# Performance work log

Hardware: AMD Instinct MI355X
Metric: run time of the kernel (lower is better)

Reference implementation:

```python
import jax, jax.numpy as jnp
import numpy as np

N_GENES = 2048   # col_dim: nodes of the PPI graph, feature dim of cols-SAGE
N_CELLS = 4096   # row_dim: nodes of the KNN graph, feature dim of rows-SAGE
E_KNN = 61440
E_PPI = 65536
INTER = 512
EMBD = 128
SLOPE = 0.01       # LeakyReLU default negative_slope
SCALE_PARAM = 3.0  # cols_encoder custom attention scale

_PARAM_SHAPES = [
    ("c0_wl", (N_GENES, N_GENES)), ("c0_wr", (N_GENES, N_GENES)), ("c0_b", (N_GENES,)),
    ("r0_wl", (N_CELLS, N_CELLS)), ("r0_wr", (N_CELLS, N_CELLS)), ("r0_b", (N_CELLS,)),
    ("c1_wl", (N_GENES, N_GENES)), ("c1_wr", (N_GENES, N_GENES)), ("c1_b", (N_GENES,)),
    ("r1_wl", (N_CELLS, N_CELLS)), ("r1_wr", (N_CELLS, N_CELLS)), ("r1_b", (N_CELLS,)),
    ("gr_w", (N_CELLS, INTER)), ("gr_b", (INTER,)),
    ("tr_wq", (INTER, EMBD)), ("tr_bq", (EMBD,)), ("tr_wk", (INTER, EMBD)), ("tr_bk", (EMBD,)),
    ("tr_wv", (INTER, EMBD)), ("tr_bv", (EMBD,)), ("tr_ws", (INTER, EMBD)), ("tr_bs", (EMBD,)),
    ("gc_w", (N_GENES, INTER)), ("gc_b", (INTER,)),
    ("tc_wq", (INTER, EMBD)), ("tc_bq", (EMBD,)), ("tc_wk", (INTER, EMBD)), ("tc_bk", (EMBD,)),
    ("tc_wv", (INTER, EMBD)), ("tc_bv", (EMBD,)), ("tc_ws", (INTER, EMBD)), ("tc_bs", (EMBD,)),
    ("d1_w", (EMBD, INTER)), ("d1_b", (INTER,)),
    ("d2_w", (INTER, INTER)), ("d2_b", (INTER,)),
    ("d3_w", (INTER, N_GENES)), ("d3_b", (N_GENES,)),
]


def setup_inputs() -> dict:
    key = jax.random.key(0)
    ki = iter(jax.random.split(key, 64))
    inp = {
        "x": jax.random.normal(next(ki), (N_GENES, N_CELLS), jnp.float32),
        "knn_edge_index": jax.random.randint(next(ki), (2, E_KNN), 0, N_CELLS, dtype=jnp.int32),
        "ppi_edge_index": jax.random.randint(next(ki), (2, E_PPI), 0, N_GENES, dtype=jnp.int32),
    }
    for name, shape in _PARAM_SHAPES:
        scale = 1.0 / float(np.sqrt(shape[0])) if len(shape) == 2 else 0.01
        inp[name] = jax.random.normal(next(ki), shape, jnp.float32) * scale
    return inp


def _leaky(x):
    return jax.nn.leaky_relu(x, SLOPE)


def _gcn(x, ei, w, b):
    # GCNConv: add self loops, symmetric D^-1/2 (A+I) D^-1/2 normalization
    n = x.shape[0]
    loop = jnp.arange(n, dtype=ei.dtype)
    src = jnp.concatenate([ei[0], loop])
    dst = jnp.concatenate([ei[1], loop])
    deg = jax.ops.segment_sum(jnp.ones(src.shape, x.dtype), dst, n)
    dinv = jnp.where(deg > 0, jax.lax.rsqrt(jnp.maximum(deg, 1.0)), 0.0)
    h = x @ w
    msg = h[src] * (dinv[src] * dinv[dst])[:, None]
    return jax.ops.segment_sum(msg, dst, n) + b


def _sage(x, ei, wl, wr, b):
    # SAGEConv: mean neighbor aggregation -> lin_l, plus root lin_r
    n = x.shape[0]
    src, dst = ei[0], ei[1]
    s = jax.ops.segment_sum(x[src], dst, n)
    cnt = jax.ops.segment_sum(jnp.ones(src.shape, x.dtype), dst, n)
    agg = s / jnp.maximum(cnt, 1.0)[:, None]
    return agg @ wl + x @ wr + b


def _tconv(x, ei, wq, bq, wk, bk, wv, bv, ws, bs, scale_param):
    # TransformerConv (heads=1). scale_param=None -> per-target softmax;
    # otherwise the custom mean/std standardization + sigmoid (TransformerConvReducrLayer).
    n, d = x.shape[0], wq.shape[1]
    q = x @ wq + bq
    k = x @ wk + bk
    v = x @ wv + bv
    src, dst = ei[0], ei[1]
    alpha = jnp.sum(q[dst] * k[src], axis=-1) / jnp.sqrt(jnp.asarray(d, x.dtype))
    if scale_param is None:
        m = jax.ops.segment_max(alpha, dst, n)
        e = jnp.exp(alpha - m[dst])
        z = jax.ops.segment_sum(e, dst, n)
        a = e / jnp.where(z > 0, z, 1.0)[dst]
    else:
        mu = jnp.mean(alpha)
        sd = jnp.std(alpha, ddof=1)  # torch.std is unbiased
        a = jax.nn.sigmoid((alpha - mu) / ((1.0 / scale_param) * sd))
    out = jax.ops.segment_sum(a[:, None] * v[src], dst, n)
    return out + x @ ws + bs  # root skip (lin_skip)


def reference(x, knn_edge_index, ppi_edge_index,
              c0_wl, c0_wr, c0_b, r0_wl, r0_wr, r0_b,
              c1_wl, c1_wr, c1_b, r1_wl, r1_wr, r1_b,
              gr_w, gr_b, tr_wq, tr_bq, tr_wk, tr_bk, tr_wv, tr_bv, tr_ws, tr_bs,
              gc_w, gc_b, tc_wq, tc_bq, tc_wk, tc_bk, tc_wv, tc_bv, tc_ws, tc_bs,
              d1_w, d1_b, d2_w, d2_b, d3_w, d3_b):
    # dropout layers are identity at inference
    emb = x  # [genes, cells]
    for (cwl, cwr, cb, rwl, rwr, rb) in [
        (c0_wl, c0_wr, c0_b, r0_wl, r0_wr, r0_b),
        (c1_wl, c1_wr, c1_b, r1_wl, r1_wr, r1_b),
    ]:
        emb = _leaky(_sage(emb.T, knn_edge_index, cwl, cwr, cb)).T  # cells graph
        emb = _leaky(_sage(emb, ppi_edge_index, rwl, rwr, rb))      # genes graph
    # rows encoder: GCN + TransformerConv (softmax attention) over PPI graph
    hr = _leaky(_gcn(emb, ppi_edge_index, gr_w, gr_b))
    emb_rows = _tconv(hr, ppi_edge_index, tr_wq, tr_bq, tr_wk, tr_bk,
                      tr_wv, tr_bv, tr_ws, tr_bs, None)
    # cols encoder: GCN + reducer TransformerConv (sigmoid-standardized attention) over KNN graph
    hc = _leaky(_gcn(emb.T, knn_edge_index, gc_w, gc_b))
    emb_cols = _tconv(hc, knn_edge_index, tc_wq, tc_bq, tc_wk, tc_bk,
                      tc_wv, tc_bv, tc_ws, tc_bs, SCALE_PARAM)
    # feature decoder MLP
    h = jax.nn.relu(emb_cols @ d1_w + d1_b)
    h = jax.nn.relu(h @ d2_w + d2_b)
    out_features = h @ d3_w + d3_b
    return (emb_rows, emb_cols, out_features)
```

## Files before the change

### kernel.cpp

```cpp
#include <hip/hip_runtime.h>
#include <math.h>

#define NG 2048
#define NC 4096
#define EKNN 61440
#define EPPI 65536

typedef __attribute__((ext_vector_type(8))) short short8v;
typedef __attribute__((ext_vector_type(4))) float f32x4;
typedef unsigned short ushort_t;

static inline int cdiv(int a, int b) { return (a + b - 1) / b; }

__device__ __forceinline__ unsigned short f2b(float f) {
    union { float f; unsigned int i; } v; v.f = f;
    unsigned int r = v.i + 0x7FFFu + ((v.i >> 16) & 1u);
    return (unsigned short)(r >> 16);
}
__device__ __forceinline__ float bl(unsigned int u) { union { unsigned int i; float f; } v; v.i = u << 16; return v.f; }
__device__ __forceinline__ float bh(unsigned int u) { union { unsigned int i; float f; } v; v.i = u & 0xFFFF0000u; return v.f; }
__device__ __forceinline__ unsigned int pk2(float a, float b) { return (unsigned int)f2b(a) | ((unsigned int)f2b(b) << 16); }

__device__ __forceinline__ int xcd_swz_id() {
    const int nwg = gridDim.x * gridDim.y;
    const int orig = blockIdx.y * gridDim.x + blockIdx.x;
    const int q = nwg >> 3, r = nwg & 7;
    const int xcd = orig & 7, off = orig >> 3;
    return (xcd < r ? xcd * (q + 1) : r * (q + 1) + (xcd - r) * q) + off;
}

#define GLOAD_LDS16(gp, lp) __builtin_amdgcn_global_load_lds( \
    (const __attribute__((address_space(1))) void*)(gp),      \
    (__attribute__((address_space(3))) void*)(lp), 16, 0, 0)

template<int ACT, bool BIAS, bool OBF>
__global__ __launch_bounds__(256)
void gemm_bf16(const ushort_t* __restrict__ A,
               const ushort_t* __restrict__ Bt,
               const float* __restrict__ bias,
               float* __restrict__ Cf, ushort_t* __restrict__ Cb,
               int M, int N, int K) {
    __shared__ ushort_t lds[2][2][128 * 32];
    const int tid = threadIdx.x;
    const int lane = tid & 63, wv = tid >> 6;
    const int wm = wv >> 1, wn = wv & 1;
    const int swzid = xcd_swz_id();
    const int bm = (swzid / gridDim.x) << 7, bn = (swzid % gridDim.x) << 7;

    const ushort_t* gA = A + (size_t)bm * K;
    const ushort_t* gB = Bt + (size_t)bn * K;

    const int rsub = lane >> 2;
    const int qsw  = (lane & 3) ^ ((lane >> 3) & 3);
    const int KT = K >> 5;

    f32x4 acc[4][4];
    #pragma unroll
    for (int i = 0; i < 4; ++i)
        #pragma unroll
        for (int j = 0; j < 4; ++j) acc[i][j] = (f32x4){0.f, 0.f, 0.f, 0.f};

    auto stage = [&](int buf, int k0) {
        #pragma unroll
        for (int t = 0; t < 2; ++t) {
            const int br = (wv * 2 + t) * 16;
            GLOAD_LDS16(gA + (size_t)(br + rsub) * K + k0 + qsw * 8, &lds[buf][0][br * 32]);
            GLOAD_LDS16(gB + (size_t)(br + rsub) * K + k0 + qsw * 8, &lds[buf][1][br * 32]);
        }
    };

    const int rl = lane & 15, kg = lane >> 4;
    const int swr = (kg ^ ((rl >> 1) & 3)) * 8;

    stage(0, 0);
    int buf = 0;
    for (int kt = 0; kt < KT; ++kt) {
        __syncthreads();
        if (kt + 1 < KT) stage(buf ^ 1, (kt + 1) << 5);
        short8v a[4], b[4];
        #pragma unroll
        for (int mi = 0; mi < 4; ++mi)
            a[mi] = *(const short8v*)&lds[buf][0][(wm * 64 + mi * 16 + rl) * 32 + swr];
        #pragma unroll
        for (int ni = 0; ni < 4; ++ni)
            b[ni] = *(const short8v*)&lds[buf][1][(wn * 64 + ni * 16 + rl) * 32 + swr];
        #pragma unroll
        for (int mi = 0; mi < 4; ++mi)
            #pragma unroll
            for (int ni = 0; ni < 4; ++ni)
                acc[mi][ni] = __builtin_amdgcn_mfma_f32_16x16x32_bf16(a[mi], b[ni], acc[mi][ni], 0, 0, 0);
        buf ^= 1;
    }

    const int colL = lane & 15, rq = lane >> 4;
    #pragma unroll
    for (int mi = 0; mi < 4; ++mi) {
        const int row0 = bm + wm * 64 + mi * 16 + rq * 4;
        #pragma unroll
        for (int ni = 0; ni < 4; ++ni) {
            const int col = bn + wn * 64 + ni * 16 + colL;
            float bv = 0.f;
            if (BIAS) bv = bias[col];
            #pragma unroll
            for (int r = 0; r < 4; ++r) {
                const size_t off = (size_t)(row0 + r) * N + col;
                float v = acc[mi][ni][r];
                if (BIAS) v += bv;
                if (ACT == 2) v = fmaxf(v, 0.f);
                if (OBF) Cb[off] = f2b(v); else Cf[off] = v;
            }
        }
    }
}

__global__ __launch_bounds__(256)
void gemm_sage(const ushort_t* __restrict__ A0, const ushort_t* __restrict__ B0t,
               const ushort_t* __restrict__ A1, const ushort_t* __restrict__ B1t,
               const float* __restrict__ bias, ushort_t* __restrict__ Cb,
               int M, int N, int K) {
    __shared__ ushort_t lds[2][2][128 * 32];
    const int tid = threadIdx.x;
    const int lane = tid & 63, wv = tid >> 6;
    const int wm = wv >> 1, wn = wv & 1;
    const int swzid = xcd_swz_id();
    const int bm = (swzid / gridDim.x) << 7, bn = (swzid % gridDim.x) << 7;

    const ushort_t* gA0 = A0 + (size_t)bm * K;
    const ushort_t* gB0 = B0t + (size_t)bn * K;
    const ushort_t* gA1 = A1 + (size_t)bm * K;
    const ushort_t* gB1 = B1t + (size_t)bn * K;

    const int rsub = lane >> 2;
    const int qsw  = (lane & 3) ^ ((lane >> 3) & 3);
    const int KT = K >> 5;

    f32x4 acc[4][4];
    #pragma unroll
    for (int i = 0; i < 4; ++i)
        #pragma unroll
        for (int j = 0; j < 4; ++j) acc[i][j] = (f32x4){0.f, 0.f, 0.f, 0.f};

    auto stage = [&](int buf, int kt) {
        const int half = kt >= KT;
        const int k0 = (half ? (kt - KT) : kt) << 5;
        const ushort_t* sA = half ? gA1 : gA0;
        const ushort_t* sB = half ? gB1 : gB0;
        #pragma unroll
        for (int t = 0; t < 2; ++t) {
            const int br = (wv * 2 + t) * 16;
            GLOAD_LDS16(sA + (size_t)(br + rsub) * K + k0 + qsw * 8, &lds[buf][0][br * 32]);
            GLOAD_LDS16(sB + (size_t)(br + rsub) * K + k0 + qsw * 8, &lds[buf][1][br * 32]);
        }
    };

    const int rl = lane & 15, kg = lane >> 4;
    const int swr = (kg ^ ((rl >> 1) & 3)) * 8;

    stage(0, 0);
    int buf = 0;
    const int KT2 = KT * 2;
    for (int kt = 0; kt < KT2; ++kt) {
        __syncthreads();
        if (kt + 1 < KT2) stage(buf ^ 1, kt + 1);
        short8v a[4], b[4];
        #pragma unroll
        for (int mi = 0; mi < 4; ++mi)
            a[mi] = *(const short8v*)&lds[buf][0][(wm * 64 + mi * 16 + rl) * 32 + swr];
        #pragma unroll
        for (int ni = 0; ni < 4; ++ni)
            b[ni] = *(const short8v*)&lds[buf][1][(wn * 64 + ni * 16 + rl) * 32 + swr];
        #pragma unroll
        for (int mi = 0; mi < 4; ++mi)
            #pragma unroll
            for (int ni = 0; ni < 4; ++ni)
                acc[mi][ni] = __builtin_amdgcn_mfma_f32_16x16x32_bf16(a[mi], b[ni], acc[mi][ni], 0, 0, 0);
        buf ^= 1;
    }

    const int colL = lane & 15, rq = lane >> 4;
    #pragma unroll
    for (int mi = 0; mi < 4; ++mi) {
        const int row0 = bm + wm * 64 + mi * 16 + rq * 4;
        float bz[4];
        #pragma unroll
        for (int r = 0; r < 4; ++r) bz[r] = bias[row0 + r];
        #pragma unroll
        for (int ni = 0; ni < 4; ++ni) {
            const int col = bn + wn * 64 + ni * 16 + colL;
            #pragma unroll
            for (int r = 0; r < 4; ++r) {
                float v = acc[mi][ni][r] + bz[r];
                v = v > 0.f ? v : 0.01f * v;
                Cb[(size_t)(row0 + r) * N + col] = f2b(v);
            }
        }
    }
}

__global__ __launch_bounds__(256)
void transpose_f2b(const float* __restrict__ in, ushort_t* __restrict__ out, int R, int C) {
    __shared__ ushort_t t[64][65];
    const int bx = blockIdx.x << 6, by = blockIdx.y << 6;
    const int tr = threadIdx.x >> 4;
    const int tc = (threadIdx.x & 15) << 2;
    #pragma unroll
    for (int i = 0; i < 4; ++i) {
        const int rr = tr + i * 16;
        const float4 v = *(const float4*)(in + (size_t)(by + rr) * C + bx + tc);
        t[rr][tc + 0] = f2b(v.x); t[rr][tc + 1] = f2b(v.y);
        t[rr][tc + 2] = f2b(v.z); t[rr][tc + 3] = f2b(v.w);
    }
    __syncthreads();
    #pragma unroll
    for (int i = 0; i < 4; ++i) {
        const int cc = tr + i * 16;
        ushort4 o;
        o.x = t[tc + 0][cc]; o.y = t[tc + 1][cc];
        o.z = t[tc + 2][cc]; o.w = t[tc + 3][cc];
        *(ushort4*)(out + (size_t)(bx + cc) * R + by + tc) = o;
    }
}

__global__ __launch_bounds__(256)
void transpose_b2b(const ushort_t* __restrict__ in, ushort_t* __restrict__ out, int R, int C) {
    __shared__ ushort_t t[64][65];
    const int bx = blockIdx.x << 6, by = blockIdx.y << 6;
    const int tr = threadIdx.x >> 4;
    const int tc = (threadIdx.x & 15) << 2;
    #pragma unroll
    for (int i = 0; i < 4; ++i) {
        const int rr = tr + i * 16;
        const ushort4 v = *(const ushort4*)(in + (size_t)(by + rr) * C + bx + tc);
        t[rr][tc + 0] = v.x; t[rr][tc + 1] = v.y;
        t[rr][tc + 2] = v.z; t[rr][tc + 3] = v.w;
    }
    __syncthreads();
    #pragma unroll
    for (int i = 0; i < 4; ++i) {
        const int cc = tr + i * 16;
        ushort4 o;
        o.x = t[tc + 0][cc]; o.y = t[tc + 1][cc];
        o.z = t[tc + 2][cc]; o.w = t[tc + 3][cc];
        *(ushort4*)(out + (size_t)(bx + cc) * R + by + tc) = o;
    }
}

__global__ __launch_bounds__(256)
void transpose_qkvs(const float* __restrict__ wq, const float* __restrict__ wk,
                    const float* __restrict__ wv, const float* __restrict__ wsk,
                    ushort_t* __restrict__ out) {
    const float* in = blockIdx.z == 0 ? wq : blockIdx.z == 1 ? wk : blockIdx.z == 2 ? wv : wsk;
    ushort_t* o = out + (size_t)blockIdx.z * 128 * 512;
    __shared__ ushort_t t[64][65];
    const int bx = blockIdx.x << 6, by = blockIdx.y << 6;
    const int tr = threadIdx.x >> 4;
    const int tc = (threadIdx.x & 15) << 2;
    #pragma unroll
    for (int i = 0; i < 4; ++i) {
        const int rr = tr + i * 16;
        const float4 v = *(const float4*)(in + (size_t)(by + rr) * 128 + bx + tc);
        t[rr][tc + 0] = f2b(v.x); t[rr][tc + 1] = f2b(v.y);
        t[rr][tc + 2] = f2b(v.z); t[rr][tc + 3] = f2b(v.w);
    }
    __syncthreads();
    #pragma unroll
    for (int i = 0; i < 4; ++i) {
        const int cc = tr + i * 16;
        ushort4 ov;
        ov.x = t[tc + 0][cc]; ov.y = t[tc + 1][cc];
        ov.z = t[tc + 2][cc]; ov.w = t[tc + 3][cc];
        *(ushort4*)(o + (size_t)(bx + cc) * 512 + by + tc) = ov;
    }
}

__global__ void count_dst(const int* __restrict__ dst, float* __restrict__ cnt, int E) {
    int e = blockIdx.x * blockDim.x + threadIdx.x;
    if (e < E) atomicAdd(&cnt[dst[e]], 1.0f);
}

__global__ void make_dinv(const float* __restrict__ cnt, float* __restrict__ dinv, int n) {
    int i = blockIdx.x * blockDim.x + threadIdx.x;
    if (i < n) dinv[i] = rsqrtf(cnt[i] + 1.0f);
}

__global__ __launch_bounds__(256)
void scan_rowptr(const float* __restrict__ cnt, int* __restrict__ rowptr, int n) {
    __shared__ int part[257];
    const int tid = threadIdx.x;
    const int per = n >> 8;
    const int base = tid * per;
    int s = 0;
    for (int i = 0; i < per; ++i) s += (int)cnt[base + i];
    part[tid + 1] = s;
    if (tid == 0) part[0] = 0;
    __syncthreads();
    if (tid == 0)
        for (int i = 1; i <= 256; ++i) part[i] += part[i - 1];
    __syncthreads();
    int run = part[tid];
    for (int i = 0; i < per; ++i) {
        rowptr[base + i] = run;
        run += (int)cnt[base + i];
    }
    if (tid == 255) rowptr[n] = run;
}

__global__ void fill_csr(const int* __restrict__ src, const int* __restrict__ dst,
                         const int* __restrict__ rowptr, int* __restrict__ cursor,
                         int* __restrict__ srcs, int* __restrict__ eids, int E) {
    int e = blockIdx.x * blockDim.x + threadIdx.x;
    if (e >= E) return;
    int d = dst[e];
    int p = atomicAdd(&cursor[d], 1);
    int idx = rowptr[d] + p;
    srcs[idx] = src[e];
    eids[idx] = e;
}

__global__ void concat4(const float* __restrict__ a, const float* __restrict__ b,
                        const float* __restrict__ c, const float* __restrict__ d,
                        float* __restrict__ o) {
    int i = threadIdx.x + blockIdx.x * blockDim.x;
    if (i >= 512) return;
    float v;
    if (i < 128) v = a[i];
    else if (i < 256) v = b[i - 128];
    else if (i < 384) v = c[i - 256];
    else v = d[i - 384];
    o[i] = v;
}

template<int NS>
__global__ __launch_bounds__(256)
void sage_gather_b(const int* __restrict__ rowptr, const int* __restrict__ srcs,
                   const ushort_t* __restrict__ x, ushort_t* __restrict__ out) {
    const int F = NS * 2048;
    const int node = blockIdx.x, tid = threadIdx.x;
    const int beg = rowptr[node], end = rowptr[node + 1];
    __shared__ int snb[256];
    float acc[NS][8];
    #pragma unroll
    for (int s = 0; s < NS; ++s)
        #pragma unroll
        for (int j = 0; j < 8; ++j) acc[s][j] = 0.f;
    for (int c = beg; c < end; c += 256) {
        const int m = min(256, end - c);
        __syncthreads();
        if (tid < m) snb[tid] = srcs[c + tid];
        __syncthreads();
        #pragma unroll 2
        for (int i = 0; i < m; ++i) {
            const uint4* row = (const uint4*)(x + (size_t)snb[i] * F);
            #pragma unroll
            for (int s = 0; s < NS; ++s) {
                const uint4 v = row[tid + s * 256];
                acc[s][0] += bl(v.x); acc[s][1] += bh(v.x);
                acc[s][2] += bl(v.y); acc[s][3] += bh(v.y);
                acc[s][4] += bl(v.z); acc[s][5] += bh(v.z);
                acc[s][6] += bl(v.w); acc[s][7] += bh(v.w);
            }
        }
    }
    const float inv = 1.f / fmaxf((float)(end - beg), 1.f);
    uint4* orow = (uint4*)(out + (size_t)node * F);
    #pragma unroll
    for (int s = 0; s < NS; ++s) {
        uint4 o;
        o.x = pk2(acc[s][0] * inv, acc[s][1] * inv);
        o.y = pk2(acc[s][2] * inv, acc[s][3] * inv);
        o.z = pk2(acc[s][4] * inv, acc[s][5] * inv);
        o.w = pk2(acc[s][6] * inv, acc[s][7] * inv);
        orow[tid + s * 256] = o;
    }
}

__global__ __launch_bounds__(128)
void gcn_gather_b(const int* __restrict__ rowptr, const int* __restrict__ srcs,
                  const float* __restrict__ h, const float* __restrict__ dinv,
                  const float* __restrict__ b, ushort_t* __restrict__ out) {
    const int node = blockIdx.x, tid = threadIdx.x;
    const int beg = rowptr[node], end = rowptr[node + 1];
    __shared__ int snb[128];
    __shared__ float sdi[128];
    float ax = 0.f, ay = 0.f, az = 0.f, aw = 0.f;
    for (int c = beg; c < end; c += 128) {
        const int m = min(128, end - c);
        __syncthreads();
        if (tid < m) { int s = srcs[c + tid]; snb[tid] = s; sdi[tid] = dinv[s]; }
        __syncthreads();
        for (int i = 0; i < m; ++i) {
            const float4 v = ((const float4*)(h + (size_t)snb[i] * 512))[tid];
            const float w = sdi[i];
            ax += v.x * w; ay += v.y * w; az += v.z * w; aw += v.w * w;
        }
    }
    const float dd = dinv[node];
    const float4 hv = ((const float4*)(h + (size_t)node * 512))[tid];
    const float4 bv = ((const float4*)b)[tid];
    float4 o;
    o.x = ax * dd + hv.x * dd * dd + bv.x;
    o.y = ay * dd + hv.y * dd * dd + bv.y;
    o.z = az * dd + hv.z * dd * dd + bv.z;
    o.w = aw * dd + hv.w * dd * dd + bv.w;
    o.x = o.x > 0.f ? o.x : 0.01f * o.x;
    o.y = o.y > 0.f ? o.y : 0.01f * o.y;
    o.z = o.z > 0.f ? o.z : 0.01f * o.z;
    o.w = o.w > 0.f ? o.w : 0.01f * o.w;
    ((uint2*)(out + (size_t)node * 512))[tid] = make_uint2(pk2(o.x, o.y), pk2(o.z, o.w));
}

__global__ __launch_bounds__(128)
void tconv_softmax_gather(const int* __restrict__ rowptr, const int* __restrict__ srcs,
                          const int* __restrict__ eids, const float* __restrict__ alpha,
                          const float* __restrict__ qkvs, float* __restrict__ out) {
    const int node = blockIdx.x, tid = threadIdx.x;
    const int beg = rowptr[node], end = rowptr[node + 1];
    __shared__ int snb[128];
    __shared__ float sa[128];
    float mx = -INFINITY;
    for (int c = beg; c < end; c += 128) {
        const int m = min(128, end - c);
        __syncthreads();
        if (tid < m) sa[tid] = alpha[eids[c + tid]];
        __syncthreads();
        for (int i = 0; i < m; ++i) mx = fmaxf(mx, sa[i]);
    }
    float acc = 0.f, z = 0.f;
    for (int c = beg; c < end; c += 128) {
        const int m = min(128, end - c);
        __syncthreads();
        if (tid < m) { snb[tid] = srcs[c + tid]; sa[tid] = __expf(alpha[eids[c + tid]] - mx); }
        __syncthreads();
        for (int i = 0; i < m; ++i) {
            z += sa[i];
            acc += sa[i] * qkvs[(size_t)snb[i] * 512 + 256 + tid];
        }
    }
    const float r = acc * (z > 0.f ? 1.f / z : 0.f) + qkvs[(size_t)node * 512 + 384 + tid];
    out[(size_t)node * 128 + tid] = r;
}

template<bool WB16>
__global__ __launch_bounds__(128)
void tconv_sigmoid_gather(const int* __restrict__ rowptr, const int* __restrict__ srcs,
                          const int* __restrict__ eids, const float* __restrict__ alpha,
                          const float* __restrict__ qkvs, const double* __restrict__ stats,
                          float scale_param, int E, float* __restrict__ out,
                          ushort_t* __restrict__ ob) {
    const int node = blockIdx.x, tid = threadIdx.x;
    const int beg = rowptr[node], end = rowptr[node + 1];
    const double sum = stats[0], sumsq = stats[1];
    const double mu = sum / (double)E;
    const double var = (sumsq - sum * sum / (double)E) / (double)(E - 1);
    const float sd = (float)sqrt(fmax(var, 0.0));
    const float kk = scale_param / sd;
    const float fmu = (float)mu;
    __shared__ int snb[128];
    __shared__ float sa[128];
    float acc = 0.f;
    for (int c = beg; c < end; c += 128) {
        const int m = min(128, end - c);
        __syncthreads();
        if (tid < m) {
            snb[tid] = srcs[c + tid];
            const float t = (alpha[eids[c + tid]] - fmu) * kk;
            sa[tid] = 1.f / (1.f + __expf(-t));
        }
        __syncthreads();
        for (int i = 0; i < m; ++i)
            acc += sa[i] * qkvs[(size_t)snb[i] * 512 + 256 + tid];
    }
    const float r = acc + qkvs[(size_t)node * 512 + 384 + tid];
    out[(size_t)node * 128 + tid] = r;
    if (WB16) ob[(size_t)node * 128 + tid] = f2b(r);
}

__global__ __launch_bounds__(256)
void edge_dot_s(const int* __restrict__ src, const int* __restrict__ dst,
                const float* __restrict__ qkvs, float* __restrict__ alpha, int E) {
    int wid = (blockIdx.x * blockDim.x + threadIdx.x) >> 6;
    int lane = threadIdx.x & 63;
    if (wid >= E) return;
    const size_t qb = (size_t)dst[wid] * 512;
    const size_t kb = (size_t)src[wid] * 512 + 128;
    float v = qkvs[qb + lane] * qkvs[kb + lane]
            + qkvs[qb + 64 + lane] * qkvs[kb + 64 + lane];
    #pragma unroll
    for (int off = 32; off; off >>= 1) v += __shfl_down(v, off);
    if (lane == 0) alpha[wid] = v * 0.08838834764831845f;
}

__global__ __launch_bounds__(256)
void reduce_stats(const float* __restrict__ a, int E, double* __restrict__ stats) {
    double s = 0.0, s2 = 0.0;
    for (int i = blockIdx.x * blockDim.x + threadIdx.x; i < E; i += gridDim.x * blockDim.x) {
        double x = a[i];
        s += x; s2 += x * x;
    }
    #pragma unroll
    for (int off = 32; off; off >>= 1) {
        s += __shfl_down(s, off);
        s2 += __shfl_down(s2, off);
    }
    __shared__ double sh[4][2];
    int w = threadIdx.x >> 6;
    if ((threadIdx.x & 63) == 0) { sh[w][0] = s; sh[w][1] = s2; }
    __syncthreads();
    if (threadIdx.x == 0) {
        double t = sh[0][0] + sh[1][0] + sh[2][0] + sh[3][0];
        double t2 = sh[0][1] + sh[1][1] + sh[2][1] + sh[3][1];
        atomicAdd(&stats[0], t);
        atomicAdd(&stats[1], t2);
    }
}

static constexpr size_t NBIG = (size_t)NG * NC;
static constexpr size_t NBH = NBIG / 2;
static constexpr size_t OFF_B1 = 0;
static constexpr size_t OFF_B2 = NBH;
static constexpr size_t OFF_B3 = 2 * NBH;
static constexpr size_t OFF_WBF = 3 * NBH;
static constexpr size_t OFF_H1   = OFF_WBF + 2097152;
static constexpr size_t OFF_H2B  = OFF_H1 + (size_t)4096 * 512;
static constexpr size_t OFF_H3B  = OFF_H2B + (size_t)4096 * 512 / 2;
static constexpr size_t OFF_QKVS = OFF_H3B + (size_t)4096 * 512 / 2;
static constexpr size_t OFF_CBF  = OFF_QKVS + (size_t)4096 * 512;
static constexpr size_t OFF_B4 = OFF_WBF + 2 * NBIG;
static constexpr size_t OFF_ALPHA = OFF_B4 + 512;
static constexpr size_t OFF_CNTK = OFF_ALPHA + 65536;
static constexpr size_t OFF_CNTP = OFF_CNTK + 4096;
static constexpr size_t OFF_DINVK = OFF_CNTP + 4096;
static constexpr size_t OFF_DINVP = OFF_DINVK + 4096;
static constexpr size_t OFF_STATS = OFF_DINVP + 4096;
static constexpr size_t OFF_RPK = OFF_STATS + 16;
static constexpr size_t OFF_RPP = OFF_RPK + 4112;
static constexpr size_t OFF_SRCK = OFF_RPP + 2064;
static constexpr size_t OFF_EIDK = OFF_SRCK + EKNN;
static constexpr size_t OFF_SRCP = OFF_EIDK + EKNN;
static constexpr size_t OFF_EIDP = OFF_SRCP + EPPI;
static constexpr size_t OFF_CUR = OFF_EIDP + EPPI;

extern "C" void kernel_launch(void* const* d_in, const int* in_sizes, int n_in,
                              void* d_out, int out_size, void* d_ws, size_t ws_size,
                              hipStream_t stream) {
    const float* x      = (const float*)d_in[0];
    const int*   knn    = (const int*)d_in[1];
    const int*   ppi    = (const int*)d_in[2];
    const float* c0_wl = (const float*)d_in[3],  *c0_wr = (const float*)d_in[4],  *c0_b = (const float*)d_in[5];
    const float* r0_wl = (const float*)d_in[6],  *r0_wr = (const float*)d_in[7],  *r0_b = (const float*)d_in[8];
    const float* c1_wl = (const float*)d_in[9],  *c1_wr = (const float*)d_in[10], *c1_b = (const float*)d_in[11];
    const float* r1_wl = (const float*)d_in[12], *r1_wr = (const float*)d_in[13], *r1_b = (const float*)d_in[14];
    const float* gr_w  = (const float*)d_in[15], *gr_b  = (const float*)d_in[16];
    const float* tr_wq = (const float*)d_in[17], *tr_bq = (const float*)d_in[18];
    const float* tr_wk = (const float*)d_in[19], *tr_bk = (const float*)d_in[20];
    const float* tr_wv = (const float*)d_in[21], *tr_bv = (const float*)d_in[22];
    const float* tr_ws = (const float*)d_in[23], *tr_bs = (const float*)d_in[24];
    const float* gc_w  = (const float*)d_in[25], *gc_b  = (const float*)d_in[26];
    const float* tc_wq = (const float*)d_in[27], *tc_bq = (const float*)d_in[28];
    const float* tc_wk = (const float*)d_in[29], *tc_bk = (const float*)d_in[30];
    const float* tc_wv = (const float*)d_in[31], *tc_bv = (const float*)d_in[32];
    const float* tc_ws = (const float*)d_in[33], *tc_bs = (const float*)d_in[34];
    const float* d1_w  = (const float*)d_in[35], *d1_b  = (const float*)d_in[36];
    const float* d2_w  = (const float*)d_in[37], *d2_b  = (const float*)d_in[38];
    const float* d3_w  = (const float*)d_in[39], *d3_b  = (const float*)d_in[40];

    const int* knn_src = knn, *knn_dst = knn + EKNN;
    const int* ppi_src = ppi, *ppi_dst = ppi + EPPI;

    float* ws = (float*)d_ws;
    ushort_t* B1 = (ushort_t*)(ws + OFF_B1);
    ushort_t* B2 = (ushort_t*)(ws + OFF_B2);
    ushort_t* B3 = (ushort_t*)(ws + OFF_B3);
    ushort_t* WBF0 = (ushort_t*)(ws + OFF_WBF);
    ushort_t* WBF1 = WBF0 + 2 * NBIG;
    float* H1 = ws + OFF_H1;
    ushort_t* H2b = (ushort_t*)(ws + OFF_H2B);
    ushort_t* H3b = (ushort_t*)(ws + OFF_H3B);
    float* QKVS = ws + OFF_QKVS;
    ushort_t* CBF = (ushort_t*)(ws + OFF_CBF);
    float* B4 = ws + OFF_B4;
    float* ALPHA = ws + OFF_ALPHA;
    float* CNTK = ws + OFF_CNTK;
    float* CNTP = ws + OFF_CNTP;
    float* DINVK = ws + OFF_DINVK;
    float* DINVP = ws + OFF_DINVP;
    double* STATS = (double*)(ws + OFF_STATS);
    int* RPK  = (int*)(ws + OFF_RPK);
    int* RPP  = (int*)(ws + OFF_RPP);
    int* SRCK = (int*)(ws + OFF_SRCK);
    int* EIDK = (int*)(ws + OFF_EIDK);
    int* SRCP = (int*)(ws + OFF_SRCP);
    int* EIDP = (int*)(ws + OFF_EIDP);
    int* CUR  = (int*)(ws + OFF_CUR);

    float* out_rows = (float*)d_out;
    float* out_cols = out_rows + (size_t)NG * 128;
    float* out_feat = out_cols + (size_t)NC * 128;

    auto tW = [&](const float* Wsrc, int K, int N, ushort_t* dst) {
        transpose_f2b<<<dim3(N >> 6, K >> 6), 256, 0, stream>>>(Wsrc, dst, K, N);
    };
    auto gemm = [&](const ushort_t* Abf, const ushort_t* Wt, const float* bias,
                    float* Cf, ushort_t* Cb, int M, int N, int K, int mode) {
        dim3 g(N >> 7, M >> 7), blk(256);
        switch (mode) {
            case 0: gemm_bf16<0, false, false><<<g, blk, 0, stream>>>(Abf, Wt, nullptr, Cf, nullptr, M, N, K); break;
            case 2: gemm_bf16<0, true,  false><<<g, blk, 0, stream>>>(Abf, Wt, bias, Cf, nullptr, M, N, K); break;
            case 3: gemm_bf16<2, true,  true ><<<g, blk, 0, stream>>>(Abf, Wt, bias, nullptr, Cb, M, N, K); break;
        }
    };

    hipMemsetAsync(CNTK, 0, NC * 4, stream);
    hipMemsetAsync(CNTP, 0, NG * 4, stream);
    count_dst<<<cdiv(EKNN, 256), 256, 0, stream>>>(knn_dst, CNTK, EKNN);
    count_dst<<<cdiv(EPPI, 256), 256, 0, stream>>>(ppi_dst, CNTP, EPPI);
    make_dinv<<<cdiv(NC, 256), 256, 0, stream>>>(CNTK, DINVK, NC);
    make_dinv<<<cdiv(NG, 256), 256, 0, stream>>>(CNTP, DINVP, NG);
    scan_rowptr<<<1, 256, 0, stream>>>(CNTK, RPK, NC);
    scan_rowptr<<<1, 256, 0, stream>>>(CNTP, RPP, NG);
    hipMemsetAsync(CUR, 0, NC * 4, stream);
    fill_csr<<<cdiv(EKNN, 256), 256, 0, stream>>>(knn_src, knn_dst, RPK, CUR, SRCK, EIDK, EKNN);
    hipMemsetAsync(CUR, 0, NG * 4, stream);
    fill_csr<<<cdiv(EPPI, 256), 256, 0, stream>>>(ppi_src, ppi_dst, RPP, CUR, SRCP, EIDP, EPPI);

    transpose_f2b<<<dim3(NC >> 6, NG >> 6), 256, 0, stream>>>(x, B1, NG, NC);
    const float* cwl[2] = {c0_wl, c1_wl}; const float* cwr[2] = {c0_wr, c1_wr}; const float* cbb[2] = {c0_b, c1_b};
    const float* rwl[2] = {r0_wl, r1_wl}; const float* rwr[2] = {r0_wr, r1_wr}; const float* rbb[2] = {r0_b, r1_b};
    for (int l = 0; l < 2; ++l) {
        sage_gather_b<1><<<NC, 256, 0, stream>>>(RPK, SRCK, B1, B2);
        tW(cwl[l], NG, NG, WBF0);
        tW(cwr[l], NG, NG, WBF1);
        gemm_sage<<<dim3(NC >> 7, NG >> 7), 256, 0, stream>>>(WBF0, B2, WBF1, B1, cbb[l], B3, NG, NC, NG);
        sage_gather_b<2><<<NG, 256, 0, stream>>>(RPP, SRCP, B3, B2);
        tW(rwl[l], NC, NC, WBF0);
        tW(rwr[l], NC, NC, WBF1);
        gemm_sage<<<dim3(NG >> 7, NC >> 7), 256, 0, stream>>>(WBF0, B2, WBF1, B3, rbb[l], B1, NC, NG, NC);
    }
    transpose_b2b<<<dim3(NG >> 6, NC >> 6), 256, 0, stream>>>(B1, B3, NC, NG);

    tW(gr_w, NC, 512, WBF0);
    gemm(B3, WBF0, nullptr, H1, nullptr, NG, 512, NC, 0);
    gcn_gather_b<<<NG, 128, 0, stream>>>(RPP, SRCP, H1, DINVP, gr_b, H2b);
    transpose_qkvs<<<dim3(2, 8, 4), 256, 0, stream>>>(tr_wq, tr_wk, tr_wv, tr_ws, WBF0);
    concat4<<<2, 256, 0, stream>>>(tr_bq, tr_bk, tr_bv, tr_bs, B4);
    gemm(H2b, WBF0, B4, QKVS, nullptr, NG, 512, 512, 2);
    edge_dot_s<<<cdiv(EPPI * 64, 256), 256, 0, stream>>>(ppi_src, ppi_dst, QKVS, ALPHA, EPPI);
    tconv_softmax_gather<<<NG, 128, 0, stream>>>(RPP, SRCP, EIDP, ALPHA, QKVS, out_rows);

    tW(gc_w, NG, 512, WBF0);
    gemm(B1, WBF0, nullptr, H1, nullptr, NC, 512, NG, 0);
    gcn_gather_b<<<NC, 128, 0, stream>>>(RPK, SRCK, H1, DINVK, gc_b, H3b);
    transpose_qkvs<<<dim3(2, 8, 4), 256, 0, stream>>>(tc_wq, tc_wk, tc_wv, tc_ws, WBF0);
    concat4<<<2, 256, 0, stream>>>(tc_bq, tc_bk, tc_bv, tc_bs, B4);
    gemm(H3b, WBF0, B4, QKVS, nullptr, NC, 512, 512, 2);
    edge_dot_s<<<cdiv(EKNN * 64, 256), 256, 0, stream>>>(knn_src, knn_dst, QKVS, ALPHA, EKNN);
    hipMemsetAsync(STATS, 0, 16, stream);
    reduce_stats<<<256, 256, 0, stream>>>(ALPHA, EKNN, STATS);
    tconv_sigmoid_gather<true><<<NC, 128, 0, stream>>>(RPK, SRCK, EIDK, ALPHA, QKVS, STATS, 3.0f, EKNN, out_cols, CBF);

    tW(d1_w, 128, 512, WBF0);
    gemm(CBF, WBF0, d1_b, nullptr, H2b, NC, 512, 128, 3);
    tW(d2_w, 512, 512, WBF0);
    gemm(H2b, WBF0, d2_b, nullptr, H3b, NC, 512, 512, 3);
    tW(d3_w, 512, NG, WBF0);
    gemm(H3b, WBF0, d3_b, out_feat, nullptr, NC, NG, 512, 2);

    (void)in_sizes; (void)n_in; (void)out_size; (void)ws_size;
}
```

Measured before the change: 1.071 ms.

## Merge rows/cols encoder branches into paired kernel launches and store GCN hidden in bf16

Launches the independent rows (PPI) and cols (KNN) encoder stages together. Graph preprocessing, the weight transposes, the GCN and QKVS GEMMs, the gathers, edge dots and attention aggregation each become one kernel that picks its branch by block index. This cuts launch count and lets small kernels fill the GPU that they underused alone. The GCN hidden buffers are now stored in bf16 rather than fp32, which halves gather traffic at some precision cost.

```diff
diff --git a/kernel.cpp b/kernel.cpp
--- a/kernel.cpp
+++ b/kernel.cpp
@@ -49,7 +49,6 @@
 
     const ushort_t* gA = A + (size_t)bm * K;
     const ushort_t* gB = Bt + (size_t)bn * K;
-
     const int rsub = lane >> 2;
     const int qsw  = (lane & 3) ^ ((lane >> 3) & 3);
     const int KT = K >> 5;
@@ -68,7 +67,6 @@
             GLOAD_LDS16(gB + (size_t)(br + rsub) * K + k0 + qsw * 8, &lds[buf][1][br * 32]);
         }
     };
-
     const int rl = lane & 15, kg = lane >> 4;
     const int swr = (kg ^ ((rl >> 1) & 3)) * 8;
 
@@ -91,7 +89,6 @@
                 acc[mi][ni] = __builtin_amdgcn_mfma_f32_16x16x32_bf16(a[mi], b[ni], acc[mi][ni], 0, 0, 0);
         buf ^= 1;
     }
-
     const int colL = lane & 15, rq = lane >> 4;
     #pragma unroll
     for (int mi = 0; mi < 4; ++mi) {
@@ -113,6 +110,93 @@
     }
 }
 
+template<bool BIAS, bool OBF>
+__global__ __launch_bounds__(256)
+void gemm2_bf16(const ushort_t* __restrict__ A0, const ushort_t* __restrict__ Bt0,
+                const float* __restrict__ bias0, float* __restrict__ Cf0, ushort_t* __restrict__ Cb0,
+                int N0, int K0, int nx0, int nb0,
+                const ushort_t* __restrict__ A1, const ushort_t* __restrict__ Bt1,
+                const float* __restrict__ bias1, float* __restrict__ Cf1, ushort_t* __restrict__ Cb1,
+                int N1, int K1, int nx1) {
+    __shared__ ushort_t lds[2][2][128 * 32];
+    const int bid = blockIdx.x;
+    const bool p1 = bid >= nb0;
+    const int lbid = p1 ? bid - nb0 : bid;
+    const ushort_t* A = p1 ? A1 : A0;
+    const ushort_t* Bt = p1 ? Bt1 : Bt0;
+    const float* bias = p1 ? bias1 : bias0;
+    float* Cf = p1 ? Cf1 : Cf0;
+    ushort_t* Cb = p1 ? Cb1 : Cb0;
+    const int N = p1 ? N1 : N0;
+    const int K = p1 ? K1 : K0;
+    const int nx = p1 ? nx1 : nx0;
+    const int bn = (lbid % nx) << 7, bm = (lbid / nx) << 7;
+
+    const int tid = threadIdx.x;
+    const int lane = tid & 63, wv = tid >> 6;
+    const int wm = wv >> 1, wn = wv & 1;
+    const ushort_t* gA = A + (size_t)bm * K;
+    const ushort_t* gB = Bt + (size_t)bn * K;
+    const int rsub = lane >> 2;
+    const int qsw  = (lane & 3) ^ ((lane >> 3) & 3);
+    const int KT = K >> 5;
+
+    f32x4 acc[4][4];
+    #pragma unroll
+    for (int i = 0; i < 4; ++i)
+        #pragma unroll
+        for (int j = 0; j < 4; ++j) acc[i][j] = (f32x4){0.f, 0.f, 0.f, 0.f};
+
+    auto stage = [&](int buf, int k0) {
+        #pragma unroll
+        for (int t = 0; t < 2; ++t) {
+            const int br = (wv * 2 + t) * 16;
+            GLOAD_LDS16(gA + (size_t)(br + rsub) * K + k0 + qsw * 8, &lds[buf][0][br * 32]);
+            GLOAD_LDS16(gB + (size_t)(br + rsub) * K + k0 + qsw * 8, &lds[buf][1][br * 32]);
+        }
+    };
+    const int rl = lane & 15, kg = lane >> 4;
+    const int swr = (kg ^ ((rl >> 1) & 3)) * 8;
+
+    stage(0, 0);
+    int buf = 0;
+    for (int kt = 0; kt < KT; ++kt) {
+        __syncthreads();
+        if (kt + 1 < KT) stage(buf ^ 1, (kt + 1) << 5);
+        short8v a[4], b[4];
+        #pragma unroll
+        for (int mi = 0; mi < 4; ++mi)
+            a[mi] = *(const short8v*)&lds[buf][0][(wm * 64 + mi * 16 + rl) * 32 + swr];
+        #pragma unroll
+        for (int ni = 0; ni < 4; ++ni)
+            b[ni] = *(const short8v*)&lds[buf][1][(wn * 64 + ni * 16 + rl) * 32 + swr];
+        #pragma unroll
+        for (int mi = 0; mi < 4; ++mi)
+            #pragma unroll
+            for (int ni = 0; ni < 4; ++ni)
+                acc[mi][ni] = __builtin_amdgcn_mfma_f32_16x16x32_bf16(a[mi], b[ni], acc[mi][ni], 0, 0, 0);
+        buf ^= 1;
+    }
+    const int colL = lane & 15, rq = lane >> 4;
+    #pragma unroll
+    for (int mi = 0; mi < 4; ++mi) {
+        const int row0 = bm + wm * 64 + mi * 16 + rq * 4;
+        #pragma unroll
+        for (int ni = 0; ni < 4; ++ni) {
+            const int col = bn + wn * 64 + ni * 16 + colL;
+            float bv = 0.f;
+            if (BIAS) bv = bias[col];
+            #pragma unroll
+            for (int r = 0; r < 4; ++r) {
+                const size_t off = (size_t)(row0 + r) * N + col;
+                float v = acc[mi][ni][r];
+                if (BIAS) v += bv;
+                if (OBF) Cb[off] = f2b(v); else Cf[off] = v;
+            }
+        }
+    }
+}
+
 __global__ __launch_bounds__(256)
 void gemm_sage(const ushort_t* __restrict__ A0, const ushort_t* __restrict__ B0t,
                const ushort_t* __restrict__ A1, const ushort_t* __restrict__ B1t,
@@ -129,7 +213,6 @@
     const ushort_t* gB0 = B0t + (size_t)bn * K;
     const ushort_t* gA1 = A1 + (size_t)bm * K;
     const ushort_t* gB1 = B1t + (size_t)bn * K;
-
     const int rsub = lane >> 2;
     const int qsw  = (lane & 3) ^ ((lane >> 3) & 3);
     const int KT = K >> 5;
@@ -152,7 +235,6 @@
             GLOAD_LDS16(sB + (size_t)(br + rsub) * K + k0 + qsw * 8, &lds[buf][1][br * 32]);
         }
     };
-
     const int rl = lane & 15, kg = lane >> 4;
     const int swr = (kg ^ ((rl >> 1) & 3)) * 8;
 
@@ -176,7 +258,6 @@
                 acc[mi][ni] = __builtin_amdgcn_mfma_f32_16x16x32_bf16(a[mi], b[ni], acc[mi][ni], 0, 0, 0);
         buf ^= 1;
     }
-
     const int colL = lane & 15, rq = lane >> 4;
     #pragma unroll
     for (int mi = 0; mi < 4; ++mi) {
@@ -222,7 +303,10 @@
 }
 
 __global__ __launch_bounds__(256)
-void transpose_b2b(const ushort_t* __restrict__ in, ushort_t* __restrict__ out, int R, int C) {
+void transpose_f2b2(const float* __restrict__ in0, ushort_t* __restrict__ out0,
+                    const float* __restrict__ in1, ushort_t* __restrict__ out1, int R, int C) {
+    const float* in = blockIdx.z ? in1 : in0;
+    ushort_t* out = blockIdx.z ? out1 : out0;
     __shared__ ushort_t t[64][65];
     const int bx = blockIdx.x << 6, by = blockIdx.y << 6;
     const int tr = threadIdx.x >> 4;
@@ -230,9 +314,9 @@
     #pragma unroll
     for (int i = 0; i < 4; ++i) {
         const int rr = tr + i * 16;
-        const ushort4 v = *(const ushort4*)(in + (size_t)(by + rr) * C + bx + tc);
-        t[rr][tc + 0] = v.x; t[rr][tc + 1] = v.y;
-        t[rr][tc + 2] = v.z; t[rr][tc + 3] = v.w;
+        const float4 v = *(const float4*)(in + (size_t)(by + rr) * C + bx + tc);
+        t[rr][tc + 0] = f2b(v.x); t[rr][tc + 1] = f2b(v.y);
+        t[rr][tc + 2] = f2b(v.z); t[rr][tc + 3] = f2b(v.w);
     }
     __syncthreads();
     #pragma unroll
@@ -246,11 +330,44 @@
 }
 
 __global__ __launch_bounds__(256)
-void transpose_qkvs(const float* __restrict__ wq, const float* __restrict__ wk,
-                    const float* __restrict__ wv, const float* __restrict__ wsk,
-                    ushort_t* __restrict__ out) {
-    const float* in = blockIdx.z == 0 ? wq : blockIdx.z == 1 ? wk : blockIdx.z == 2 ? wv : wsk;
-    ushort_t* o = out + (size_t)blockIdx.z * 128 * 512;
+void transpose_b2b(const ushort_t* __restrict__ in, ushort_t* __restrict__ out, int R, int C) {
+    __shared__ ushort_t t[64][65];
+    const int bx = blockIdx.x << 6, by = blockIdx.y << 6;
+    const int tr = threadIdx.x >> 4;
+    const int tc = (threadIdx.x & 15) << 2;
+    #pragma unroll
+    for (int i = 0; i < 4; ++i) {
+        const int rr = tr + i * 16;
+        const ushort4 v = *(const ushort4*)(in + (size_t)(by + rr) * C + bx + tc);
+        t[rr][tc + 0] = v.x; t[rr][tc + 1] = v.y;
+        t[rr][tc + 2] = v.z; t[rr][tc + 3] = v.w;
+    }
+    __syncthreads();
+    #pragma unroll
+    for (int i = 0; i < 4; ++i) {
+        const int cc = tr + i * 16;
+        ushort4 o;
+        o.x = t[tc + 0][cc]; o.y = t[tc + 1][cc];
+        o.z = t[tc + 2][cc]; o.w = t[tc + 3][cc];
+        *(ushort4*)(out + (size_t)(bx + cc) * R + by + tc) = o;
+    }
+}
+
+__global__ __launch_bounds__(256)
+void transpose_qkvs8(const float* __restrict__ w0, const float* __restrict__ w1,
+                     const float* __restrict__ w2, const float* __restrict__ w3,
+                     const float* __restrict__ w4, const float* __restrict__ w5,
+                     const float* __restrict__ w6, const float* __restrict__ w7,
+                     ushort_t* __restrict__ outR, ushort_t* __restrict__ outC) {
+    const int z = blockIdx.z;
+    const float* in;
+    switch (z) {
+        case 0: in = w0; break; case 1: in = w1; break;
+        case 2: in = w2; break; case 3: in = w3; break;
+        case 4: in = w4; break; case 5: in = w5; break;
+        case 6: in = w6; break; default: in = w7; break;
+    }
+    ushort_t* o = (z < 4 ? outR + (size_t)z * 128 * 512 : outC + (size_t)(z - 4) * 128 * 512);
     __shared__ ushort_t t[64][65];
     const int bx = blockIdx.x << 6, by = blockIdx.y << 6;
     const int tr = threadIdx.x >> 4;
@@ -273,18 +390,26 @@
     }
 }
 
-__global__ void count_dst(const int* __restrict__ dst, float* __restrict__ cnt, int E) {
+__global__ void count_dst2(const int* __restrict__ pdst, float* __restrict__ cntp,
+                           const int* __restrict__ kdst, float* __restrict__ cntk) {
     int e = blockIdx.x * blockDim.x + threadIdx.x;
-    if (e < E) atomicAdd(&cnt[dst[e]], 1.0f);
-}
-
-__global__ void make_dinv(const float* __restrict__ cnt, float* __restrict__ dinv, int n) {
+    if (e < EPPI) atomicAdd(&cntp[pdst[e]], 1.0f);
+    else if (e < EPPI + EKNN) atomicAdd(&cntk[kdst[e - EPPI]], 1.0f);
+}
+
+__global__ void make_dinv2(const float* __restrict__ cntp, float* __restrict__ dinvp,
+                           const float* __restrict__ cntk, float* __restrict__ dinvk) {
     int i = blockIdx.x * blockDim.x + threadIdx.x;
-    if (i < n) dinv[i] = rsqrtf(cnt[i] + 1.0f);
-}
-
-__global__ __launch_bounds__(256)
-void scan_rowptr(const float* __restrict__ cnt, int* __restrict__ rowptr, int n) {
+    if (i < NG) dinvp[i] = rsqrtf(cntp[i] + 1.0f);
+    else if (i < NG + NC) dinvk[i - NG] = rsqrtf(cntk[i - NG] + 1.0f);
+}
+
+__global__ __launch_bounds__(256)
+void scan_rowptr2(const float* __restrict__ cntp, int* __restrict__ rpp,
+                  const float* __restrict__ cntk, int* __restrict__ rpk) {
+    const float* cnt = blockIdx.x ? cntk : cntp;
+    int* rowptr = blockIdx.x ? rpk : rpp;
+    const int n = blockIdx.x ? NC : NG;
     __shared__ int part[257];
     const int tid = threadIdx.x;
     const int per = n >> 8;
@@ -305,29 +430,41 @@
     if (tid == 255) rowptr[n] = run;
 }
 
-__global__ void fill_csr(const int* __restrict__ src, const int* __restrict__ dst,
-                         const int* __restrict__ rowptr, int* __restrict__ cursor,
-                         int* __restrict__ srcs, int* __restrict__ eids, int E) {
+__global__ void fill_csr2(const int* __restrict__ psrc, const int* __restrict__ pdst,
+                          const int* __restrict__ rpp, int* __restrict__ curp,
+                          int* __restrict__ srcp, int* __restrict__ eidp,
+                          const int* __restrict__ ksrc, const int* __restrict__ kdst,
+                          const int* __restrict__ rpk, int* __restrict__ curk,
+                          int* __restrict__ srck, int* __restrict__ eidk) {
     int e = blockIdx.x * blockDim.x + threadIdx.x;
-    if (e >= E) return;
-    int d = dst[e];
-    int p = atomicAdd(&cursor[d], 1);
-    int idx = rowptr[d] + p;
-    srcs[idx] = src[e];
-    eids[idx] = e;
-}
-
-__global__ void concat4(const float* __restrict__ a, const float* __restrict__ b,
+    if (e < EPPI) {
+        int d = pdst[e];
+        int p = atomicAdd(&curp[d], 1);
+        srcp[rpp[d] + p] = psrc[e];
+        eidp[rpp[d] + p] = e;
+    } else if (e < EPPI + EKNN) {
+        int e2 = e - EPPI;
+        int d = kdst[e2];
+        int p = atomicAdd(&curk[d], 1);
+        srck[rpk[d] + p] = ksrc[e2];
+        eidk[rpk[d] + p] = e2;
+    }
+}
+
+__global__ void concat8(const float* __restrict__ a, const float* __restrict__ b,
                         const float* __restrict__ c, const float* __restrict__ d,
+                        const float* __restrict__ e, const float* __restrict__ f,
+                        const float* __restrict__ g, const float* __restrict__ h,
                         float* __restrict__ o) {
     int i = threadIdx.x + blockIdx.x * blockDim.x;
-    if (i >= 512) return;
-    float v;
-    if (i < 128) v = a[i];
-    else if (i < 256) v = b[i - 128];
-    else if (i < 384) v = c[i - 256];
-    else v = d[i - 384];
-    o[i] = v;
+    if (i >= 1024) return;
+    const float* s;
+    int j = i & 127;
+    switch (i >> 7) {
+        case 0: s = a; break; case 1: s = b; break; case 2: s = c; break; case 3: s = d; break;
+        case 4: s = e; break; case 5: s = f; break; case 6: s = g; break; default: s = h; break;
+    }
+    o[i] = s[j];
 }
 
 template<int NS>
@@ -375,10 +512,22 @@
 }
 
 __global__ __launch_bounds__(128)
-void gcn_gather_b(const int* __restrict__ rowptr, const int* __restrict__ srcs,
-                  const float* __restrict__ h, const float* __restrict__ dinv,
-                  const float* __restrict__ b, ushort_t* __restrict__ out) {
-    const int node = blockIdx.x, tid = threadIdx.x;
+void gcn_gather2(const int* __restrict__ rpp, const int* __restrict__ srcp,
+                 const ushort_t* __restrict__ hr, const float* __restrict__ dinvp,
+                 const float* __restrict__ br, ushort_t* __restrict__ outr,
+                 const int* __restrict__ rpk, const int* __restrict__ srck,
+                 const ushort_t* __restrict__ hc, const float* __restrict__ dinvk,
+                 const float* __restrict__ bc, ushort_t* __restrict__ outc) {
+    const bool cols = blockIdx.x >= NG;
+    const int node = cols ? blockIdx.x - NG : blockIdx.x;
+    const int tid = threadIdx.x;
+    const int* rowptr = cols ? rpk : rpp;
+    const int* srcs = cols ? srck : srcp;
+    const ushort_t* h = cols ? hc : hr;
+    const float* dinv = cols ? dinvk : dinvp;
+    const float* b = cols ? bc : br;
+    ushort_t* out = cols ? outc : outr;
+
     const int beg = rowptr[node], end = rowptr[node + 1];
     __shared__ int snb[128];
     __shared__ float sdi[128];
@@ -389,19 +538,20 @@
         if (tid < m) { int s = srcs[c + tid]; snb[tid] = s; sdi[tid] = dinv[s]; }
         __syncthreads();
         for (int i = 0; i < m; ++i) {
-            const float4 v = ((const float4*)(h + (size_t)snb[i] * 512))[tid];
+            const uint2 v = ((const uint2*)(h + (size_t)snb[i] * 512))[tid];
             const float w = sdi[i];
-            ax += v.x * w; ay += v.y * w; az += v.z * w; aw += v.w * w;
+            ax += bl(v.x) * w; ay += bh(v.x) * w;
+            az += bl(v.y) * w; aw += bh(v.y) * w;
         }
     }
     const float dd = dinv[node];
-    const float4 hv = ((const float4*)(h + (size_t)node * 512))[tid];
+    const uint2 hv = ((const uint2*)(h + (size_t)node * 512))[tid];
     const float4 bv = ((const float4*)b)[tid];
     float4 o;
-    o.x = ax * dd + hv.x * dd * dd + bv.x;
-    o.y = ay * dd + hv.y * dd * dd + bv.y;
-    o.z = az * dd + hv.z * dd * dd + bv.z;
-    o.w = aw * dd + hv.w * dd * dd + bv.w;
+    o.x = ax * dd + bl(hv.x) * dd * dd + bv.x;
+    o.y = ay * dd + bh(hv.x) * dd * dd + bv.y;
+    o.z = az * dd + bl(hv.y) * dd * dd + bv.z;
+    o.w = aw * dd + bh(hv.y) * dd * dd + bv.w;
     o.x = o.x > 0.f ? o.x : 0.01f * o.x;
     o.y = o.y > 0.f ? o.y : 0.01f * o.y;
     o.z = o.z > 0.f ? o.z : 0.01f * o.z;
@@ -409,85 +559,27 @@
     ((uint2*)(out + (size_t)node * 512))[tid] = make_uint2(pk2(o.x, o.y), pk2(o.z, o.w));
 }
 
-__global__ __launch_bounds__(128)
-void tconv_softmax_gather(const int* __restrict__ rowptr, const int* __restrict__ srcs,
-                          const int* __restrict__ eids, const float* __restrict__ alpha,
-                          const float* __restrict__ qkvs, float* __restrict__ out) {
-    const int node = blockIdx.x, tid = threadIdx.x;
-    const int beg = rowptr[node], end = rowptr[node + 1];
-    __shared__ int snb[128];
-    __shared__ float sa[128];
-    float mx = -INFINITY;
-    for (int c = beg; c < end; c += 128) {
-        const int m = min(128, end - c);
-        __syncthreads();
-        if (tid < m) sa[tid] = alpha[eids[c + tid]];
-        __syncthreads();
-        for (int i = 0; i < m; ++i) mx = fmaxf(mx, sa[i]);
-    }
-    float acc = 0.f, z = 0.f;
-    for (int c = beg; c < end; c += 128) {
-        const int m = min(128, end - c);
-        __syncthreads();
-        if (tid < m) { snb[tid] = srcs[c + tid]; sa[tid] = __expf(alpha[eids[c + tid]] - mx); }
-        __syncthreads();
-        for (int i = 0; i < m; ++i) {
-            z += sa[i];
-            acc += sa[i] * qkvs[(size_t)snb[i] * 512 + 256 + tid];
-        }
-    }
-    const float r = acc * (z > 0.f ? 1.f / z : 0.f) + qkvs[(size_t)node * 512 + 384 + tid];
-    out[(size_t)node * 128 + tid] = r;
-}
-
-template<bool WB16>
-__global__ __launch_bounds__(128)
-void tconv_sigmoid_gather(const int* __restrict__ rowptr, const int* __restrict__ srcs,
-                          const int* __restrict__ eids, const float* __restrict__ alpha,
-                          const float* __restrict__ qkvs, const double* __restrict__ stats,
-                          float scale_param, int E, float* __restrict__ out,
-                          ushort_t* __restrict__ ob) {
-    const int node = blockIdx.x, tid = threadIdx.x;
-    const int beg = rowptr[node], end = rowptr[node + 1];
-    const double sum = stats[0], sumsq = stats[1];
-    const double mu = sum / (double)E;
-    const double var = (sumsq - sum * sum / (double)E) / (double)(E - 1);
-    const float sd = (float)sqrt(fmax(var, 0.0));
-    const float kk = scale_param / sd;
-    const float fmu = (float)mu;
-    __shared__ int snb[128];
-    __shared__ float sa[128];
-    float acc = 0.f;
-    for (int c = beg; c < end; c += 128) {
-        const int m = min(128, end - c);
-        __syncthreads();
-        if (tid < m) {
-            snb[tid] = srcs[c + tid];
-            const float t = (alpha[eids[c + tid]] - fmu) * kk;
-            sa[tid] = 1.f / (1.f + __expf(-t));
-        }
-        __syncthreads();
-        for (int i = 0; i < m; ++i)
-            acc += sa[i] * qkvs[(size_t)snb[i] * 512 + 256 + tid];
-    }
-    const float r = acc + qkvs[(size_t)node * 512 + 384 + tid];
-    out[(size_t)node * 128 + tid] = r;
-    if (WB16) ob[(size_t)node * 128 + tid] = f2b(r);
-}
-
-__global__ __launch_bounds__(256)
-void edge_dot_s(const int* __restrict__ src, const int* __restrict__ dst,
-                const float* __restrict__ qkvs, float* __restrict__ alpha, int E) {
+__global__ __launch_bounds__(256)
+void edge_dot2(const int* __restrict__ psrc, const int* __restrict__ pdst,
+               const float* __restrict__ qr, float* __restrict__ alphap,
+               const int* __restrict__ ksrc, const int* __restrict__ kdst,
+               const float* __restrict__ qc, float* __restrict__ alphak) {
     int wid = (blockIdx.x * blockDim.x + threadIdx.x) >> 6;
     int lane = threadIdx.x & 63;
-    if (wid >= E) return;
-    const size_t qb = (size_t)dst[wid] * 512;
-    const size_t kb = (size_t)src[wid] * 512 + 128;
-    float v = qkvs[qb + lane] * qkvs[kb + lane]
-            + qkvs[qb + 64 + lane] * qkvs[kb + 64 + lane];
+    const float* q;
+    float* out;
+    int s, d, w;
+    if (wid < EPPI) {
+        w = wid; s = psrc[w]; d = pdst[w]; q = qr; out = alphap;
+    } else if (wid < EPPI + EKNN) {
+        w = wid - EPPI; s = ksrc[w]; d = kdst[w]; q = qc; out = alphak;
+    } else return;
+    const size_t qb = (size_t)d * 512;
+    const size_t kb = (size_t)s * 512 + 128;
+    float v = q[qb + lane] * q[kb + lane] + q[qb + 64 + lane] * q[kb + 64 + lane];
     #pragma unroll
     for (int off = 32; off; off >>= 1) v += __shfl_down(v, off);
-    if (lane == 0) alpha[wid] = v * 0.08838834764831845f;
+    if (lane == 0) out[w] = v * 0.08838834764831845f;
 }
 
 __global__ __launch_bounds__(256)
@@ -514,31 +606,102 @@
     }
 }
 
+__global__ __launch_bounds__(128)
+void tconv2(const int* __restrict__ rpp, const int* __restrict__ srcp,
+            const int* __restrict__ eidp, const float* __restrict__ alphap,
+            const float* __restrict__ qr, float* __restrict__ outr,
+            const int* __restrict__ rpk, const int* __restrict__ srck,
+            const int* __restrict__ eidk, const float* __restrict__ alphak,
+            const float* __restrict__ qc, const double* __restrict__ stats,
+            float* __restrict__ outc, ushort_t* __restrict__ ob) {
+    const int tid = threadIdx.x;
+    __shared__ int snb[128];
+    __shared__ float sa[128];
+    if (blockIdx.x < NG) {
+        const int node = blockIdx.x;
+        const int beg = rpp[node], end = rpp[node + 1];
+        float mx = -INFINITY;
+        for (int c = beg; c < end; c += 128) {
+            const int m = min(128, end - c);
+            __syncthreads();
+            if (tid < m) sa[tid] = alphap[eidp[c + tid]];
+            __syncthreads();
+            for (int i = 0; i < m; ++i) mx = fmaxf(mx, sa[i]);
+        }
+        float acc = 0.f, z = 0.f;
+        for (int c = beg; c < end; c += 128) {
+            const int m = min(128, end - c);
+            __syncthreads();
+            if (tid < m) { snb[tid] = srcp[c + tid]; sa[tid] = __expf(alphap[eidp[c + tid]] - mx); }
+            __syncthreads();
+            for (int i = 0; i < m; ++i) {
+                z += sa[i];
+                acc += sa[i] * qr[(size_t)snb[i] * 512 + 256 + tid];
+            }
+        }
+        const float r = acc * (z > 0.f ? 1.f / z : 0.f) + qr[(size_t)node * 512 + 384 + tid];
+        outr[(size_t)node * 128 + tid] = r;
+    } else {
+        const int node = blockIdx.x - NG;
+        const int beg = rpk[node], end = rpk[node + 1];
+        const double sum = stats[0], sumsq = stats[1];
+        const double mu = sum / (double)EKNN;
+        const double var = (sumsq - sum * sum / (double)EKNN) / (double)(EKNN - 1);
+        const float sd = (float)sqrt(fmax(var, 0.0));
+        const float kk = 3.0f / sd;
+        const float fmu = (float)mu;
+        float acc = 0.f;
+        for (int c = beg; c < end; c += 128) {
+            const int m = min(128, end - c);
+            __syncthreads();
+            if (tid < m) {
+                snb[tid] = srck[c + tid];
+                const float t = (alphak[eidk[c + tid]] - fmu) * kk;
+                sa[tid] = 1.f / (1.f + __expf(-t));
+            }
+            __syncthreads();
+            for (int i = 0; i < m; ++i)
+                acc += sa[i] * qc[(size_t)snb[i] * 512 + 256 + tid];
+        }
+        const float r = acc + qc[(size_t)node * 512 + 384 + tid];
+        outc[(size_t)node * 128 + tid] = r;
+        ob[(size_t)node * 128 + tid] = f2b(r);
+    }
+}
+
 static constexpr size_t NBIG = (size_t)NG * NC;
 static constexpr size_t NBH = NBIG / 2;
 static constexpr size_t OFF_B1 = 0;
 static constexpr size_t OFF_B2 = NBH;
 static constexpr size_t OFF_B3 = 2 * NBH;
 static constexpr size_t OFF_WBF = 3 * NBH;
-static constexpr size_t OFF_H1   = OFF_WBF + 2097152;
-static constexpr size_t OFF_H2B  = OFF_H1 + (size_t)4096 * 512;
-static constexpr size_t OFF_H3B  = OFF_H2B + (size_t)4096 * 512 / 2;
-static constexpr size_t OFF_QKVS = OFF_H3B + (size_t)4096 * 512 / 2;
-static constexpr size_t OFF_CBF  = OFF_QKVS + (size_t)4096 * 512;
-static constexpr size_t OFF_B4 = OFF_WBF + 2 * NBIG;
-static constexpr size_t OFF_ALPHA = OFF_B4 + 512;
-static constexpr size_t OFF_CNTK = OFF_ALPHA + 65536;
-static constexpr size_t OFF_CNTP = OFF_CNTK + 4096;
-static constexpr size_t OFF_DINVK = OFF_CNTP + 4096;
-static constexpr size_t OFF_DINVP = OFF_DINVK + 4096;
-static constexpr size_t OFF_STATS = OFF_DINVP + 4096;
-static constexpr size_t OFF_RPK = OFF_STATS + 16;
-static constexpr size_t OFF_RPP = OFF_RPK + 4112;
-static constexpr size_t OFF_SRCK = OFF_RPP + 2064;
+static constexpr size_t OFF_OV   = OFF_WBF + 2097152;
+static constexpr size_t OFF_HRB  = OFF_OV;
+static constexpr size_t OFF_HCB  = OFF_HRB + 524288;
+static constexpr size_t OFF_H2B  = OFF_HCB + 1048576;
+static constexpr size_t OFF_H3B  = OFF_H2B + 524288;
+static constexpr size_t OFF_QKVSR = OFF_H3B + 1048576;
+static constexpr size_t OFF_QKVSC = OFF_QKVSR + 1048576;
+static constexpr size_t OFF_CBF  = OFF_QKVSC + 2097152;
+static constexpr size_t OFF_WQR  = OFF_CBF + 262144;
+static constexpr size_t OFF_WQC  = OFF_WQR + 131072;
+static constexpr size_t OFF_D1T  = OFF_WQC + 131072;
+static constexpr size_t OFF_D2T  = OFF_D1T + 32768;
+static constexpr size_t OFF_D3T  = OFF_D2T + 131072;
+static constexpr size_t OFF_TAIL = OFF_WBF + 2 * NBIG;
+static constexpr size_t OFF_B4   = OFF_TAIL;
+static constexpr size_t OFF_ALPHAP = OFF_B4 + 1024;
+static constexpr size_t OFF_ALPHAK = OFF_ALPHAP + EPPI;
+static constexpr size_t OFF_CNT  = OFF_ALPHAK + EKNN;
+static constexpr size_t OFF_DINVP = OFF_CNT + 12288;
+static constexpr size_t OFF_DINVK = OFF_DINVP + NG;
+static constexpr size_t OFF_STATS = OFF_DINVK + NC;
+static constexpr size_t OFF_RPP  = OFF_STATS + 16;
+static constexpr size_t OFF_RPK  = OFF_RPP + 2064;
+static constexpr size_t OFF_SRCP = OFF_RPK + 4112;
+static constexpr size_t OFF_EIDP = OFF_SRCP + EPPI;
+static constexpr size_t OFF_SRCK = OFF_EIDP + EPPI;
 static constexpr size_t OFF_EIDK = OFF_SRCK + EKNN;
-static constexpr size_t OFF_SRCP = OFF_EIDK + EKNN;
-static constexpr size_t OFF_EIDP = OFF_SRCP + EPPI;
-static constexpr size_t OFF_CUR = OFF_EIDP + EPPI;
 
 extern "C" void kernel_launch(void* const* d_in, const int* in_sizes, int n_in,
                               void* d_out, int out_size, void* d_ws, size_t ws_size,
@@ -573,25 +736,36 @@
     ushort_t* B3 = (ushort_t*)(ws + OFF_B3);
     ushort_t* WBF0 = (ushort_t*)(ws + OFF_WBF);
     ushort_t* WBF1 = WBF0 + 2 * NBIG;
-    float* H1 = ws + OFF_H1;
-    ushort_t* H2b = (ushort_t*)(ws + OFF_H2B);
-    ushort_t* H3b = (ushort_t*)(ws + OFF_H3B);
-    float* QKVS = ws + OFF_QKVS;
+    ushort_t* GRT = WBF0;
+    ushort_t* GCT = WBF0 + 2097152;
+    ushort_t* HRB = (ushort_t*)(ws + OFF_HRB);
+    ushort_t* HCB = (ushort_t*)(ws + OFF_HCB);
+    ushort_t* H2B = (ushort_t*)(ws + OFF_H2B);
+    ushort_t* H3B = (ushort_t*)(ws + OFF_H3B);
+    float* QKVSR = ws + OFF_QKVSR;
+    float* QKVSC = ws + OFF_QKVSC;
     ushort_t* CBF = (ushort_t*)(ws + OFF_CBF);
+    ushort_t* WQR = (ushort_t*)(ws + OFF_WQR);
+    ushort_t* WQC = (ushort_t*)(ws + OFF_WQC);
+    ushort_t* D1T = (ushort_t*)(ws + OFF_D1T);
+    ushort_t* D2T = (ushort_t*)(ws + OFF_D2T);
+    ushort_t* D3T = (ushort_t*)(ws + OFF_D3T);
     float* B4 = ws + OFF_B4;
-    float* ALPHA = ws + OFF_ALPHA;
-    float* CNTK = ws + OFF_CNTK;
-    float* CNTP = ws + OFF_CNTP;
+    float* ALPHAP = ws + OFF_ALPHAP;
+    float* ALPHAK = ws + OFF_ALPHAK;
+    float* CNTP = ws + OFF_CNT;
+    float* CNTK = CNTP + NG;
+    int* CURP = (int*)(CNTK + NC);
+    int* CURK = CURP + NG;
+    float* DINVP = ws + OFF_DINVP;
     float* DINVK = ws + OFF_DINVK;
-    float* DINVP = ws + OFF_DINVP;
     double* STATS = (double*)(ws + OFF_STATS);
+    int* RPP  = (int*)(ws + OFF_RPP);
     int* RPK  = (int*)(ws + OFF_RPK);
-    int* RPP  = (int*)(ws + OFF_RPP);
+    int* SRCP = (int*)(ws + OFF_SRCP);
+    int* EIDP = (int*)(ws + OFF_EIDP);
     int* SRCK = (int*)(ws + OFF_SRCK);
     int* EIDK = (int*)(ws + OFF_EIDK);
-    int* SRCP = (int*)(ws + OFF_SRCP);
-    int* EIDP = (int*)(ws + OFF_EIDP);
-    int* CUR  = (int*)(ws + OFF_CUR);
 
     float* out_rows = (float*)d_out;
     float* out_cols = out_rows + (size_t)NG * 128;
@@ -604,66 +778,57 @@
                     float* Cf, ushort_t* Cb, int M, int N, int K, int mode) {
         dim3 g(N >> 7, M >> 7), blk(256);
         switch (mode) {
-            case 0: gemm_bf16<0, false, false><<<g, blk, 0, stream>>>(Abf, Wt, nullptr, Cf, nullptr, M, N, K); break;
             case 2: gemm_bf16<0, true,  false><<<g, blk, 0, stream>>>(Abf, Wt, bias, Cf, nullptr, M, N, K); break;
             case 3: gemm_bf16<2, true,  true ><<<g, blk, 0, stream>>>(Abf, Wt, bias, nullptr, Cb, M, N, K); break;
         }
     };
 
-    hipMemsetAsync(CNTK, 0, NC * 4, stream);
-    hipMemsetAsync(CNTP, 0, NG * 4, stream);
-    count_dst<<<cdiv(EKNN, 256), 256, 0, stream>>>(knn_dst, CNTK, EKNN);
-    count_dst<<<cdiv(EPPI, 256), 256, 0, stream>>>(ppi_dst, CNTP, EPPI);
-    make_dinv<<<cdiv(NC, 256), 256, 0, stream>>>(CNTK, DINVK, NC);
-    make_dinv<<<cdiv(NG, 256), 256, 0, stream>>>(CNTP, DINVP, NG);
-    scan_rowptr<<<1, 256, 0, stream>>>(CNTK, RPK, NC);
-    scan_rowptr<<<1, 256, 0, stream>>>(CNTP, RPP, NG);
-    hipMemsetAsync(CUR, 0, NC * 4, stream);
-    fill_csr<<<cdiv(EKNN, 256), 256, 0, stream>>>(knn_src, knn_dst, RPK, CUR, SRCK, EIDK, EKNN);
-    hipMemsetAsync(CUR, 0, NG * 4, stream);
-    fill_csr<<<cdiv(EPPI, 256), 256, 0, stream>>>(ppi_src, ppi_dst, RPP, CUR, SRCP, EIDP, EPPI);
+    hipMemsetAsync(CNTP, 0, 12288 * 4, stream);
+    count_dst2<<<cdiv(EPPI + EKNN, 256), 256, 0, stream>>>(ppi_dst, CNTP, knn_dst, CNTK);
+    make_dinv2<<<cdiv(NG + NC, 256), 256, 0, stream>>>(CNTP, DINVP, CNTK, DINVK);
+    scan_rowptr2<<<2, 256, 0, stream>>>(CNTP, RPP, CNTK, RPK);
+    fill_csr2<<<cdiv(EPPI + EKNN, 256), 256, 0, stream>>>(ppi_src, ppi_dst, RPP, CURP, SRCP, EIDP,
+                                                          knn_src, knn_dst, RPK, CURK, SRCK, EIDK);
 
     transpose_f2b<<<dim3(NC >> 6, NG >> 6), 256, 0, stream>>>(x, B1, NG, NC);
     const float* cwl[2] = {c0_wl, c1_wl}; const float* cwr[2] = {c0_wr, c1_wr}; const float* cbb[2] = {c0_b, c1_b};
     const float* rwl[2] = {r0_wl, r1_wl}; const float* rwr[2] = {r0_wr, r1_wr}; const float* rbb[2] = {r0_b, r1_b};
     for (int l = 0; l < 2; ++l) {
         sage_gather_b<1><<<NC, 256, 0, stream>>>(RPK, SRCK, B1, B2);
-        tW(cwl[l], NG, NG, WBF0);
-        tW(cwr[l], NG, NG, WBF1);
+        transpose_f2b2<<<dim3(NG >> 6, NG >> 6, 2), 256, 0, stream>>>(cwl[l], WBF0, cwr[l], WBF1, NG, NG);
         gemm_sage<<<dim3(NC >> 7, NG >> 7), 256, 0, stream>>>(WBF0, B2, WBF1, B1, cbb[l], B3, NG, NC, NG);
         sage_gather_b<2><<<NG, 256, 0, stream>>>(RPP, SRCP, B3, B2);
-        tW(rwl[l], NC, NC, WBF0);
-        tW(rwr[l], NC, NC, WBF1);
+        transpose_f2b2<<<dim3(NC >> 6, NC >> 6, 2), 256, 0, stream>>>(rwl[l], WBF0, rwr[l], WBF1, NC, NC);
         gemm_sage<<<dim3(NG >> 7, NC >> 7), 256, 0, stream>>>(WBF0, B2, WBF1, B3, rbb[l], B1, NC, NG, NC);
     }
     transpose_b2b<<<dim3(NG >> 6, NC >> 6), 256, 0, stream>>>(B1, B3, NC, NG);
 
-    tW(gr_w, NC, 512, WBF0);
-    gemm(B3, WBF0, nullptr, H1, nullptr, NG, 512, NC, 0);
-    gcn_gather_b<<<NG, 128, 0, stream>>>(RPP, SRCP, H1, DINVP, gr_b, H2b);
-    transpose_qkvs<<<dim3(2, 8, 4), 256, 0, stream>>>(tr_wq, tr_wk, tr_wv, tr_ws, WBF0);
-    concat4<<<2, 256, 0, stream>>>(tr_bq, tr_bk, tr_bv, tr_bs, B4);
-    gemm(H2b, WBF0, B4, QKVS, nullptr, NG, 512, 512, 2);
-    edge_dot_s<<<cdiv(EPPI * 64, 256), 256, 0, stream>>>(ppi_src, ppi_dst, QKVS, ALPHA, EPPI);
-    tconv_softmax_gather<<<NG, 128, 0, stream>>>(RPP, SRCP, EIDP, ALPHA, QKVS, out_rows);
-
-    tW(gc_w, NG, 512, WBF0);
-    gemm(B1, WBF0, nullptr, H1, nullptr, NC, 512, NG, 0);
-    gcn_gather_b<<<NC, 128, 0, stream>>>(RPK, SRCK, H1, DINVK, gc_b, H3b);
-    transpose_qkvs<<<dim3(2, 8, 4), 256, 0, stream>>>(tc_wq, tc_wk, tc_wv, tc_ws, WBF0);
-    concat4<<<2, 256, 0, stream>>>(tc_bq, tc_bk, tc_bv, tc_bs, B4);
-    gemm(H3b, WBF0, B4, QKVS, nullptr, NC, 512, 512, 2);
-    edge_dot_s<<<cdiv(EKNN * 64, 256), 256, 0, stream>>>(knn_src, knn_dst, QKVS, ALPHA, EKNN);
+    tW(gr_w, NC, 512, GRT);
+    tW(gc_w, NG, 512, GCT);
+    gemm2_bf16<false, true><<<64 + 128, 256, 0, stream>>>(
+        B3, GRT, nullptr, nullptr, HRB, 512, NC, 4, 64,
+        B1, GCT, nullptr, nullptr, HCB, 512, NG, 4);
+    gcn_gather2<<<NG + NC, 128, 0, stream>>>(RPP, SRCP, HRB, DINVP, gr_b, H2B,
+                                             RPK, SRCK, HCB, DINVK, gc_b, H3B);
+    transpose_qkvs8<<<dim3(2, 8, 8), 256, 0, stream>>>(tr_wq, tr_wk, tr_wv, tr_ws,
+                                                       tc_wq, tc_wk, tc_wv, tc_ws, WQR, WQC);
+    concat8<<<4, 256, 0, stream>>>(tr_bq, tr_bk, tr_bv, tr_bs, tc_bq, tc_bk, tc_bv, tc_bs, B4);
+    gemm2_bf16<true, false><<<64 + 128, 256, 0, stream>>>(
+        H2B, WQR, B4, QKVSR, nullptr, 512, 512, 4, 64,
+        H3B, WQC, B4 + 512, QKVSC, nullptr, 512, 512, 4);
+    edge_dot2<<<cdiv((EPPI + EKNN) * 64, 256), 256, 0, stream>>>(
+        ppi_src, ppi_dst, QKVSR, ALPHAP, knn_src, knn_dst, QKVSC, ALPHAK);
     hipMemsetAsync(STATS, 0, 16, stream);
-    reduce_stats<<<256, 256, 0, stream>>>(ALPHA, EKNN, STATS);
-    tconv_sigmoid_gather<true><<<NC, 128, 0, stream>>>(RPK, SRCK, EIDK, ALPHA, QKVS, STATS, 3.0f, EKNN, out_cols, CBF);
-
-    tW(d1_w, 128, 512, WBF0);
-    gemm(CBF, WBF0, d1_b, nullptr, H2b, NC, 512, 128, 3);
-    tW(d2_w, 512, 512, WBF0);
-    gemm(H2b, WBF0, d2_b, nullptr, H3b, NC, 512, 512, 3);
-    tW(d3_w, 512, NG, WBF0);
-    gemm(H3b, WBF0, d3_b, out_feat, nullptr, NC, NG, 512, 2);
+    reduce_stats<<<256, 256, 0, stream>>>(ALPHAK, EKNN, STATS);
+    tconv2<<<NG + NC, 128, 0, stream>>>(RPP, SRCP, EIDP, ALPHAP, QKVSR, out_rows,
+                                        RPK, SRCK, EIDK, ALPHAK, QKVSC, STATS, out_cols, CBF);
+
+    tW(d1_w, 128, 512, D1T);
+    gemm(CBF, D1T, d1_b, nullptr, H2B, NC, 512, 128, 3);
+    tW(d2_w, 512, 512, D2T);
+    gemm(H2B, D2T, d2_b, nullptr, H3B, NC, 512, 512, 3);
+    tW(d3_w, 512, NG, D3T);
+    gemm(H3B, D3T, d3_b, out_feat, nullptr, NC, NG, 512, 2);
 
     (void)in_sizes; (void)n_in; (void)out_size; (void)ws_size;
 }
```

After: 974.8 us. 9.0% less time.
